# Performance work log

Hardware: AMD Instinct MI355X
Metric: run time of the kernel (lower is better)

Reference implementation:

```python
import jax, jax.numpy as jnp
import numpy as np

J, XD, HD, YD, P, N = 64, 512, 1024, 16, 8, 1024


def setup_inputs() -> dict:
    key = jax.random.key(0)
    ks = jax.random.split(key, 14)
    b1 = 2.0 / np.sqrt(XD)
    b2 = 2.0 / np.sqrt(HD)
    rng = np.random.RandomState(0)
    # stack of P permutation matrices [P, YD, YD]
    permu = jnp.asarray(np.stack([np.eye(YD, dtype=np.float32)[rng.permutation(YD)] for _ in range(P)]))
    return {
        "x": jax.random.normal(ks[0], (N, XD), jnp.float32),
        "mu_W1": b1 * (jax.random.uniform(ks[1], (XD, HD)) - 0.5),
        "mu_b1": b1 * (jax.random.uniform(ks[2], (1, HD)) - 0.5),
        "mu_W2": b2 * (jax.random.uniform(ks[3], (HD, YD)) - 0.5),
        "mu_b2": b2 * (jax.random.uniform(ks[4], (1, YD)) - 0.5),
        "sig_W1": b1 * jax.random.uniform(ks[5], (XD, HD)),
        "sig_b1": b1 * jax.random.uniform(ks[6], (1, HD)),
        "sig_W2": b2 * jax.random.uniform(ks[7], (HD, YD)),
        "sig_b2": b2 * jax.random.uniform(ks[8], (1, YD)),
        "e_W1": jax.random.normal(ks[9], (J, XD, HD), jnp.float32),
        "e_b1": jax.random.normal(ks[10], (J, 1, HD), jnp.float32),
        "e_W2": jax.random.normal(ks[11], (J, HD, YD), jnp.float32),
        "e_b2": jax.random.normal(ks[12], (J, 1, YD), jnp.float32),
        "permu": permu,
    }


def reference(x, mu_W1, mu_b1, mu_W2, mu_b2, sig_W1, sig_b1, sig_W2, sig_b2,
              e_W1, e_b1, e_W2, e_b2, permu):
    # reparameterized weight samples: [J, ...]
    W1 = mu_W1 + e_W1 * sig_W1          # [J, XD, HD]
    b1 = mu_b1 + e_b1 * sig_b1          # [J, 1, HD]
    W2 = mu_W2 + e_W2 * sig_W2          # [J, HD, YD]
    b2 = mu_b2 + e_b2 * sig_b2          # [J, 1, YD]
    xf = x.reshape(-1, XD)
    # Hardtanh(-1, 1) == clip
    h = jnp.clip(jnp.einsum('nx,jxh->jnh', xf, W1) + b1, -1.0, 1.0)  # [J, N, HD]
    out = jnp.einsum('jnh,jhy->jny', h, W2) + b2                      # [J, N, YD]
    all_out = jnp.einsum('jnc,pcy->jpny', out, permu)                 # [J, P, N, YD]
    return all_out.reshape(J * P, xf.shape[0], YD)
```

## Files before the change

kernel.cpp:

```cpp
#include <hip/hip_runtime.h>
#include <cstdint>
#include <cstddef>

#define J 64
#define XD 512
#define HD 1024
#define YD 16
#define PP 8
#define NN 1024

typedef __bf16 bf16;
typedef __attribute__((ext_vector_type(8))) __bf16 bf16x8;
typedef __attribute__((ext_vector_type(4))) __bf16 bf16x4;
typedef __attribute__((ext_vector_type(4))) float f32x4;


__device__ __forceinline__ void gload16(const void* g, void* l) {
  __builtin_amdgcn_global_load_lds((__attribute__((address_space(1))) void*)(g),
                                   (__attribute__((address_space(3))) void*)(l),
                                   16, 0, 0);
}

__global__ __launch_bounds__(256) void build_w1t(
    const float* __restrict__ muW1, const float* __restrict__ sigW1,
    const float* __restrict__ eW1, bf16* __restrict__ W1T) {
  __shared__ bf16 sT[64][66];
  int b = blockIdx.x;
  int j = b >> 7;
  int xt = (b >> 4) & 7;
  int ht = b & 15;
  int x0 = xt << 6, h0 = ht << 6;
  int tid = threadIdx.x;
  int rp = tid >> 4;
  int cp = (tid & 15) << 2;
  const float* eB = eW1 + (size_t)j * (XD * HD);
#pragma unroll
  for (int p = 0; p < 4; ++p) {
    int x = rp + (p << 4);
    size_t gi = (size_t)(x0 + x) * HD + (h0 + cp);
    f32x4 e = *(const f32x4*)(eB + gi);
    f32x4 m = *(const f32x4*)(muW1 + gi);
    f32x4 s = *(const f32x4*)(sigW1 + gi);
#pragma unroll
    for (int i = 0; i < 4; ++i) sT[cp + i][x] = (bf16)(m[i] + e[i] * s[i]);
  }
  __syncthreads();
#pragma unroll
  for (int p = 0; p < 4; ++p) {
    int h = rp + (p << 4);
    bf16x4 v;
#pragma unroll
    for (int i = 0; i < 4; ++i) v[i] = sT[h][cp + i];
    *(bf16x4*)(W1T + (size_t)(j * HD + h0 + h) * XD + (x0 + cp)) = v;
  }
}

__global__ __launch_bounds__(256) void build_small(
    const float* __restrict__ x,
    const float* __restrict__ muW2, const float* __restrict__ sigW2,
    const float* __restrict__ eW2,
    const float* __restrict__ mub1, const float* __restrict__ sigb1,
    const float* __restrict__ eb1,
    const float* __restrict__ mub2, const float* __restrict__ sigb2,
    const float* __restrict__ eb2,
    bf16* __restrict__ XBF, bf16* __restrict__ W2T,
    float* __restrict__ B1W, float* __restrict__ B2W) {
  int i = blockIdx.x * 256 + threadIdx.x;
  const int c0 = NN * XD;
  const int c1 = J * YD * HD;
  const int c2 = J * HD;
  const int c3 = J * YD;
  if (i < c0) { XBF[i] = (bf16)x[i]; return; }
  i -= c0;
  if (i < c1) {
    int h = i & (HD - 1);
    int jy = i >> 10;
    int y = jy & 15;
    int j = jy >> 4;
    float mu = muW2[h * YD + y], sg = sigW2[h * YD + y];
    float e = eW2[((size_t)j * HD + h) * YD + y];
    W2T[i] = (bf16)(mu + e * sg);
    return;
  }
  i -= c1;
  if (i < c2) {
    int h = i & (HD - 1);
    B1W[i] = mub1[h] + eb1[i] * sigb1[h];
    return;
  }
  i -= c2;
  if (i < c3) {
    int y = i & 15;
    B2W[i] = mub2[y] + eb2[i] * sigb2[y];
  }
}

__global__ __launch_bounds__(256, 2) void fused_mlp(
    const bf16* __restrict__ XBF, const bf16* __restrict__ W1T,
    const bf16* __restrict__ W2T, const float* __restrict__ B1W,
    const float* __restrict__ B2W, const float* __restrict__ permu,
    float* __restrict__ out) {
  extern __shared__ char smem[];
  bf16* sA = (bf16*)smem;
  bf16* sB = (bf16*)(smem + 16384);
  bf16* sH = (bf16*)(smem + 32768);
  float* sOut = (float*)smem;
  int* sIdx = (int*)(smem + 16384);

  int b = blockIdx.x;
  int L = ((b & 7) << 6) + (b >> 3);
  int j = L >> 3;
  int n0 = (L & 7) << 7;

  int tid = threadIdx.x;
  int wid = tid >> 6;
  int lane = tid & 63;
  int l15 = lane & 15;
  int lg = lane >> 4;
  int wr = (wid >> 1) << 6;
  int wc = (wid & 1) << 6;
  int srow = (wid << 3) + (lane >> 3);
  int sslot = lane & 7;

  f32x4 acc2[2];
#pragma unroll
  for (int f = 0; f < 2; ++f)
#pragma unroll
    for (int r = 0; r < 4; ++r) acc2[f][r] = 0.0f;

  const bf16* w1base = W1T + (size_t)j * HD * XD;
  const bf16* w2g = W2T + (size_t)((j << 4) + l15) * HD;

#pragma unroll 1
  for (int hb = 0; hb < HD / 128; ++hb) {
    f32x4 acc1[4][4];
#pragma unroll
    for (int fa = 0; fa < 4; ++fa)
#pragma unroll
      for (int fb = 0; fb < 4; ++fb)
#pragma unroll
        for (int r = 0; r < 4; ++r) acc1[fa][fb][r] = 0.0f;

#pragma unroll 1
    for (int ks = 0; ks < XD / 64; ++ks) {
      int k0 = ks << 6;
      __syncthreads();
#pragma unroll
      for (int p = 0; p < 4; ++p) {
        int r = (p << 5) + srow;
        int sc = sslot ^ (r & 7);
        gload16(XBF + (size_t)(n0 + r) * XD + k0 + (sc << 3),
                (char*)sA + (p << 12) + (wid << 10));
        gload16(w1base + (size_t)((hb << 7) + r) * XD + k0 + (sc << 3),
                (char*)sB + (p << 12) + (wid << 10));
      }
      __syncthreads();
#pragma unroll
      for (int kk = 0; kk < 2; ++kk) {
        bf16x8 af[4], bg[4];
#pragma unroll
        for (int f = 0; f < 4; ++f) {
          int ra = wr + (f << 4) + l15;
          int ca = ((kk << 6) + (lg << 4)) ^ ((ra & 7) << 4);
          af[f] = *(const bf16x8*)((char*)sA + (ra << 7) + ca);
          int rb = wc + (f << 4) + l15;
          int cb = ((kk << 6) + (lg << 4)) ^ ((rb & 7) << 4);
          bg[f] = *(const bf16x8*)((char*)sB + (rb << 7) + cb);
        }
#pragma unroll
        for (int fa = 0; fa < 4; ++fa)
#pragma unroll
          for (int fb = 0; fb < 4; ++fb)
            acc1[fa][fb] = __builtin_amdgcn_mfma_f32_16x16x32_bf16(
                af[fa], bg[fb], acc1[fa][fb], 0, 0, 0);
      }
    }
    float b1v[4];
#pragma unroll
    for (int fb = 0; fb < 4; ++fb)
      b1v[fb] = B1W[j * HD + (hb << 7) + wc + (fb << 4) + l15];
#pragma unroll
    for (int fa = 0; fa < 4; ++fa) {
#pragma unroll
      for (int fb = 0; fb < 4; ++fb) {
        int col = wc + (fb << 4) + l15;
#pragma unroll
        for (int r = 0; r < 4; ++r) {
          int row = wr + (fa << 4) + (lg << 2) + r;
          float v = acc1[fa][fb][r] + b1v[fb];
          v = fminf(1.0f, fmaxf(-1.0f, v));
          int byte = (row << 8) + (((col << 1)) ^ ((row & 7) << 4));
          *(bf16*)((char*)sH + byte) = (bf16)v;
        }
      }
    }
    __syncthreads();
#pragma unroll
    for (int kk = 0; kk < 4; ++kk) {
      bf16x8 wg = *(const bf16x8*)(w2g + (hb << 7) + (kk << 5) + (lg << 3));
#pragma unroll
      for (int f = 0; f < 2; ++f) {
        int row = (wid << 5) + (f << 4) + l15;
        int cb = ((kk << 6) + (lg << 4)) ^ ((row & 7) << 4);
        bf16x8 hf = *(const bf16x8*)((char*)sH + (row << 8) + cb);
        acc2[f] = __builtin_amdgcn_mfma_f32_16x16x32_bf16(hf, wg, acc2[f], 0, 0, 0);
      }
    }
  }
  float b2v = B2W[(j << 4) + l15];
#pragma unroll
  for (int f = 0; f < 2; ++f)
#pragma unroll
    for (int r = 0; r < 4; ++r) {
      int row = (wid << 5) + (f << 4) + (lg << 2) + r;
      sOut[row * 17 + l15] = acc2[f][r] + b2v;
    }
  if (tid < 128) {
    int p = tid >> 4, y = tid & 15;
    int c = 0;
#pragma unroll
    for (int cc = 0; cc < 16; ++cc)
      if (permu[((p << 4) + cc) * 16 + y] > 0.5f) c = cc;
    sIdx[tid] = c;
  }
  __syncthreads();
#pragma unroll 1
  for (int it = 0; it < 16; ++it) {
    int flat = (it << 10) + (tid << 2);
    int p = flat >> 11;
    int n = (flat >> 4) & 127;
    int y0 = flat & 15;
    f32x4 v;
#pragma unroll
    for (int q = 0; q < 4; ++q) v[q] = sOut[n * 17 + sIdx[(p << 4) + y0 + q]];
    *(f32x4*)(out + ((size_t)((j << 3) + p) * NN + n0 + n) * YD + y0) = v;
  }
}

extern "C" void kernel_launch(void* const* d_in, const int* in_sizes, int n_in,
                              void* d_out, int out_size, void* d_ws, size_t ws_size,
                              hipStream_t stream) {
  (void)in_sizes; (void)n_in; (void)out_size; (void)ws_size;
  const float* x      = (const float*)d_in[0];
  const float* mu_W1  = (const float*)d_in[1];
  const float* mu_b1  = (const float*)d_in[2];
  const float* mu_W2  = (const float*)d_in[3];
  const float* mu_b2  = (const float*)d_in[4];
  const float* sig_W1 = (const float*)d_in[5];
  const float* sig_b1 = (const float*)d_in[6];
  const float* sig_W2 = (const float*)d_in[7];
  const float* sig_b2 = (const float*)d_in[8];
  const float* e_W1   = (const float*)d_in[9];
  const float* e_b1   = (const float*)d_in[10];
  const float* e_W2   = (const float*)d_in[11];
  const float* e_b2   = (const float*)d_in[12];
  const float* permu  = (const float*)d_in[13];
  float* out = (float*)d_out;

  char* ws = (char*)d_ws;
  bf16* W1T = (bf16*)(ws);
  bf16* W2T = (bf16*)(ws + 67108864);
  bf16* XBF = (bf16*)(ws + 69206016);
  float* B1W = (float*)(ws + 70254592);
  float* B2W = (float*)(ws + 70516736);

  build_w1t<<<dim3(8192), dim3(256), 0, stream>>>(mu_W1, sig_W1, e_W1, W1T);
  build_small<<<dim3(6404), dim3(256), 0, stream>>>(
      x, mu_W2, sig_W2, e_W2, mu_b1, sig_b1, e_b1, mu_b2, sig_b2, e_b2,
      XBF, W2T, B1W, B2W);
  fused_mlp<<<dim3(512), dim3(256), 65536, stream>>>(
      XBF, W1T, W2T, B1W, B2W, permu, out);
}
```

Before: 127.7 us.

## Enlarge fused MLP tiles to 256x256 with double-buffered async LDS loads

The fused MLP kernel now runs 512-thread blocks over 256-row by 256-hidden tiles, halving the grid to 256 blocks. It double-buffers the X and W1 tiles in LDS so global-to-LDS loads for the next k-step overlap the MFMA work on the current one. The H tile goes through LDS in four chunks, one per warp column group. This reuses each loaded tile across more MFMAs and hides load latency, at the cost of 160KB of LDS per block, more barriers in the second-layer stage, and only one block per CU across 256 CUs.

```diff
diff --git a/kernel.cpp b/kernel.cpp
--- a/kernel.cpp
+++ b/kernel.cpp
@@ -95,32 +95,30 @@
   }
 }
 
-__global__ __launch_bounds__(256, 2) void fused_mlp(
+__global__ __launch_bounds__(512, 2) void fused_mlp(
     const bf16* __restrict__ XBF, const bf16* __restrict__ W1T,
     const bf16* __restrict__ W2T, const float* __restrict__ B1W,
     const float* __restrict__ B2W, const float* __restrict__ permu,
     float* __restrict__ out) {
   extern __shared__ char smem[];
-  bf16* sA = (bf16*)smem;
-  bf16* sB = (bf16*)(smem + 16384);
-  bf16* sH = (bf16*)(smem + 32768);
-  float* sOut = (float*)smem;
-  int* sIdx = (int*)(smem + 16384);
-
-  int b = blockIdx.x;
-  int L = ((b & 7) << 6) + (b >> 3);
-  int j = L >> 3;
-  int n0 = (L & 7) << 7;
+
+  int bid = blockIdx.x;
+  int j = ((bid & 7) << 3) | (bid >> 5);
+  int n0 = ((bid >> 3) & 3) << 8;
 
   int tid = threadIdx.x;
   int wid = tid >> 6;
   int lane = tid & 63;
   int l15 = lane & 15;
   int lg = lane >> 4;
-  int wr = (wid >> 1) << 6;
-  int wc = (wid & 1) << 6;
-  int srow = (wid << 3) + (lane >> 3);
-  int sslot = lane & 7;
+  int wn = (wid >> 2) << 7;
+  int wh = (wid & 3) << 6;
+  int srow = tid >> 3;
+  int slot = tid & 7;
+
+  const bf16* w1base = W1T + (size_t)j * (HD * XD);
+  const bf16* w2g = W2T + (size_t)((j << 4) + l15) * HD;
+  bf16* sH = (bf16*)(smem + 131072);
 
   f32x4 acc2[2];
 #pragma unroll
@@ -128,86 +126,108 @@
 #pragma unroll
     for (int r = 0; r < 4; ++r) acc2[f][r] = 0.0f;
 
-  const bf16* w1base = W1T + (size_t)j * HD * XD;
-  const bf16* w2g = W2T + (size_t)((j << 4) + l15) * HD;
+  auto stage = [&](int d, int k0, int hb_) {
+    char* aD = smem + d * 32768 + (tid << 4);
+    char* bD = smem + 65536 + d * 32768 + (tid << 4);
+#pragma unroll
+    for (int q = 0; q < 4; ++q) {
+      int r = (q << 6) + srow;
+      int sc = slot ^ (r & 7);
+      gload16(XBF + (size_t)(n0 + r) * XD + k0 + (sc << 3), aD + (q << 13));
+      gload16(w1base + (size_t)((hb_ << 8) + r) * XD + k0 + (sc << 3), bD + (q << 13));
+    }
+  };
+
+  stage(0, 0, 0);
+  asm volatile("s_waitcnt vmcnt(0)" ::: "memory");
+  __builtin_amdgcn_s_barrier();
 
 #pragma unroll 1
-  for (int hb = 0; hb < HD / 128; ++hb) {
-    f32x4 acc1[4][4];
-#pragma unroll
-    for (int fa = 0; fa < 4; ++fa)
+  for (int hb = 0; hb < 4; ++hb) {
+    f32x4 acc1[8][4];
+#pragma unroll
+    for (int fa = 0; fa < 8; ++fa)
 #pragma unroll
       for (int fb = 0; fb < 4; ++fb)
 #pragma unroll
         for (int r = 0; r < 4; ++r) acc1[fa][fb][r] = 0.0f;
 
+    int cur = 0;
 #pragma unroll 1
-    for (int ks = 0; ks < XD / 64; ++ks) {
-      int k0 = ks << 6;
-      __syncthreads();
-#pragma unroll
-      for (int p = 0; p < 4; ++p) {
-        int r = (p << 5) + srow;
-        int sc = sslot ^ (r & 7);
-        gload16(XBF + (size_t)(n0 + r) * XD + k0 + (sc << 3),
-                (char*)sA + (p << 12) + (wid << 10));
-        gload16(w1base + (size_t)((hb << 7) + r) * XD + k0 + (sc << 3),
-                (char*)sB + (p << 12) + (wid << 10));
-      }
-      __syncthreads();
+    for (int t = 0; t < 8; ++t) {
+      if (t < 7)            stage(cur ^ 1, (t + 1) << 6, hb);
+      else if (hb < 3)      stage(cur ^ 1, 0, hb + 1);
+      const char* a_d = smem + cur * 32768;
+      const char* b_d = smem + 65536 + cur * 32768;
 #pragma unroll
       for (int kk = 0; kk < 2; ++kk) {
-        bf16x8 af[4], bg[4];
-#pragma unroll
-        for (int f = 0; f < 4; ++f) {
-          int ra = wr + (f << 4) + l15;
+        bf16x8 af[8], bg[4];
+#pragma unroll
+        for (int fa = 0; fa < 8; ++fa) {
+          int ra = wn + (fa << 4) + l15;
           int ca = ((kk << 6) + (lg << 4)) ^ ((ra & 7) << 4);
-          af[f] = *(const bf16x8*)((char*)sA + (ra << 7) + ca);
-          int rb = wc + (f << 4) + l15;
+          af[fa] = *(const bf16x8*)(a_d + (ra << 7) + ca);
+        }
+#pragma unroll
+        for (int fb = 0; fb < 4; ++fb) {
+          int rb = wh + (fb << 4) + l15;
           int cb = ((kk << 6) + (lg << 4)) ^ ((rb & 7) << 4);
-          bg[f] = *(const bf16x8*)((char*)sB + (rb << 7) + cb);
+          bg[fb] = *(const bf16x8*)(b_d + (rb << 7) + cb);
         }
 #pragma unroll
-        for (int fa = 0; fa < 4; ++fa)
+        for (int fa = 0; fa < 8; ++fa)
 #pragma unroll
           for (int fb = 0; fb < 4; ++fb)
             acc1[fa][fb] = __builtin_amdgcn_mfma_f32_16x16x32_bf16(
                 af[fa], bg[fb], acc1[fa][fb], 0, 0, 0);
       }
+      asm volatile("s_waitcnt vmcnt(0)" ::: "memory");
+      __builtin_amdgcn_s_barrier();
+      cur ^= 1;
     }
+
     float b1v[4];
 #pragma unroll
     for (int fb = 0; fb < 4; ++fb)
-      b1v[fb] = B1W[j * HD + (hb << 7) + wc + (fb << 4) + l15];
-#pragma unroll
-    for (int fa = 0; fa < 4; ++fa) {
-#pragma unroll
-      for (int fb = 0; fb < 4; ++fb) {
-        int col = wc + (fb << 4) + l15;
-#pragma unroll
-        for (int r = 0; r < 4; ++r) {
-          int row = wr + (fa << 4) + (lg << 2) + r;
-          float v = acc1[fa][fb][r] + b1v[fb];
-          v = fminf(1.0f, fmaxf(-1.0f, v));
-          int byte = (row << 8) + (((col << 1)) ^ ((row & 7) << 4));
-          *(bf16*)((char*)sH + byte) = (bf16)v;
+      b1v[fb] = B1W[(j << 10) + (hb << 8) + wh + (fb << 4) + l15];
+
+#pragma unroll 1
+    for (int c = 0; c < 4; ++c) {
+      __syncthreads();
+      if ((wid & 3) == c) {
+#pragma unroll
+        for (int fa = 0; fa < 8; ++fa)
+#pragma unroll
+          for (int fb = 0; fb < 4; ++fb) {
+            int col = (fb << 4) + l15;
+#pragma unroll
+            for (int r = 0; r < 4; ++r) {
+              int row = wn + (fa << 4) + (lg << 2) + r;
+              float v = acc1[fa][fb][r] + b1v[fb];
+              v = fminf(1.0f, fmaxf(-1.0f, v));
+              int byte = (row << 7) + (((col << 1)) ^ ((row & 7) << 4));
+              *(bf16*)((char*)sH + byte) = (bf16)v;
+            }
+          }
+      }
+      __syncthreads();
+#pragma unroll
+      for (int kk2 = 0; kk2 < 2; ++kk2) {
+        bf16x8 wg = *(const bf16x8*)(w2g + (hb << 8) + (c << 6) + (kk2 << 5) + (lg << 3));
+#pragma unroll
+        for (int f = 0; f < 2; ++f) {
+          int row = (wid << 5) + (f << 4) + l15;
+          int cb = ((kk2 << 6) + (lg << 4)) ^ ((row & 7) << 4);
+          bf16x8 hf = *(const bf16x8*)((char*)sH + (row << 7) + cb);
+          acc2[f] = __builtin_amdgcn_mfma_f32_16x16x32_bf16(hf, wg, acc2[f], 0, 0, 0);
         }
       }
     }
-    __syncthreads();
-#pragma unroll
-    for (int kk = 0; kk < 4; ++kk) {
-      bf16x8 wg = *(const bf16x8*)(w2g + (hb << 7) + (kk << 5) + (lg << 3));
-#pragma unroll
-      for (int f = 0; f < 2; ++f) {
-        int row = (wid << 5) + (f << 4) + l15;
-        int cb = ((kk << 6) + (lg << 4)) ^ ((row & 7) << 4);
-        bf16x8 hf = *(const bf16x8*)((char*)sH + (row << 8) + cb);
-        acc2[f] = __builtin_amdgcn_mfma_f32_16x16x32_bf16(hf, wg, acc2[f], 0, 0, 0);
-      }
-    }
-  }
+  }
+
   float b2v = B2W[(j << 4) + l15];
+  float* sOut = (float*)smem;
+  int* sIdx = (int*)(smem + 20480);
 #pragma unroll
   for (int f = 0; f < 2; ++f)
 #pragma unroll
@@ -226,9 +246,9 @@
   __syncthreads();
 #pragma unroll 1
   for (int it = 0; it < 16; ++it) {
-    int flat = (it << 10) + (tid << 2);
-    int p = flat >> 11;
-    int n = (flat >> 4) & 127;
+    int flat = (it << 11) + (tid << 2);
+    int p = flat >> 12;
+    int n = (flat >> 4) & 255;
     int y0 = flat & 15;
     f32x4 v;
 #pragma unroll
@@ -264,10 +284,17 @@
   float* B1W = (float*)(ws + 70254592);
   float* B2W = (float*)(ws + 70516736);
 
+  static int lds_set = 0;
+  if (!lds_set) {
+    hipFuncSetAttribute((const void*)fused_mlp,
+                        hipFuncAttributeMaxDynamicSharedMemorySize, 163840);
+    lds_set = 1;
+  }
+
   build_w1t<<<dim3(8192), dim3(256), 0, stream>>>(mu_W1, sig_W1, e_W1, W1T);
   build_small<<<dim3(6404), dim3(256), 0, stream>>>(
       x, mu_W2, sig_W2, e_W2, mu_b1, sig_b1, e_b1, mu_b2, sig_b2, e_b2,
       XBF, W2T, B1W, B2W);
-  fused_mlp<<<dim3(512), dim3(256), 65536, stream>>>(
+  fused_mlp<<<dim3(256), dim3(512), 163840, stream>>>(
       XBF, W1T, W2T, B1W, B2W, permu, out);
 }
```

Measured after the change: 174.4 us. 1.37x slower.
